# Kernel optimization log

Measured on AMD Instinct MI355X. Metric: run time of the kernel, lower is better.

Reference implementation:

```python
import jax, jax.numpy as jnp
import numpy as np

B, CIN, COUT, K, S, P, D = 4, 128, 128, 3, 1, 1, 1
H = W = 96
MASK_SCALE = 2.0


def setup_inputs() -> dict:
    key = jax.random.key(0)
    k1, k2, k3, k4 = jax.random.split(key, 4)
    x = jax.random.normal(k1, (B, CIN, H, W), jnp.float32)
    weight = jax.random.normal(k2, (COUT, CIN, K, K), jnp.float32) * 0.05
    bias = jax.random.normal(k3, (COUT,), jnp.float32) * 0.05
    # conv_offset_mask: out_channels = deformable_groups*3*K*K = 27, no bias
    w_offmask = jax.random.normal(k4, (3 * K * K, CIN, K, K), jnp.float32) * 0.01
    return {"x": x, "weight": weight, "bias": bias, "w_offmask": w_offmask}


def _bilinear_gather(x, py, px):
    """x: [B,C,H,W]; py,px: [B,K2,Ho,Wo] float sample coords.
    Returns [B,C,K2,Ho,Wo], zero outside image (per-corner validity as in DCNv2)."""
    Bn, C, Hh, Ww = x.shape
    K2, Ho, Wo = py.shape[1], py.shape[2], py.shape[3]
    y0 = jnp.floor(py); x0 = jnp.floor(px)
    ly = py - y0; lx = px - x0
    y0i = y0.astype(jnp.int32); x0i = x0.astype(jnp.int32)
    y1i = y0i + 1; x1i = x0i + 1
    x_flat = x.reshape(Bn, C, Hh * Ww)

    def corner(yi, xi, w):
        valid = (yi >= 0) & (yi < Hh) & (xi >= 0) & (xi < Ww)
        yc = jnp.clip(yi, 0, Hh - 1)
        xc = jnp.clip(xi, 0, Ww - 1)
        idx = (yc * Ww + xc).reshape(Bn, K2 * Ho * Wo)
        v = jnp.take_along_axis(x_flat, idx[:, None, :], axis=2)  # [B,C,K2*Ho*Wo]
        v = v.reshape(Bn, C, K2, Ho, Wo)
        wv = (w * valid.astype(x.dtype))[:, None]  # [B,1,K2,Ho,Wo]
        return v * wv

    out = corner(y0i, x0i, (1 - ly) * (1 - lx))
    out = out + corner(y0i, x1i, (1 - ly) * lx)
    out = out + corner(y1i, x0i, ly * (1 - lx))
    out = out + corner(y1i, x1i, ly * lx)
    return out


def reference(x, weight, bias, w_offmask):
    K2 = K * K
    # offset/mask conv (standard conv, no bias)
    om = jax.lax.conv_general_dilated(
        x, w_offmask, window_strides=(S, S), padding=[(P, P), (P, P)],
        dimension_numbers=("NCHW", "OIHW", "NCHW"))  # [B, 3*K2, Ho, Wo]
    o1 = om[:, :K2]
    o2 = om[:, K2:2 * K2]
    mask = jax.nn.sigmoid(om[:, 2 * K2:]) * MASK_SCALE  # [B,K2,Ho,Wo]
    offset = jnp.concatenate([o1, o2], axis=1)  # [B,2*K2,Ho,Wo]

    Ho, Wo = om.shape[2], om.shape[3]
    ki, kj = jnp.meshgrid(jnp.arange(K), jnp.arange(K), indexing="ij")
    ki = ki.reshape(K2); kj = kj.reshape(K2)
    ho = jnp.arange(Ho); wo = jnp.arange(Wo)
    base_y = (ho[None, :] * S - P + ki[:, None] * D).astype(x.dtype)  # [K2,Ho]
    base_x = (wo[None, :] * S - P + kj[:, None] * D).astype(x.dtype)  # [K2,Wo]
    py = base_y[None, :, :, None] + o1  # [B,K2,Ho,Wo]
    px = base_x[None, :, None, :] + o2

    sampled = _bilinear_gather(x, py, px)            # [B,C,K2,Ho,Wo]
    sampled = sampled * mask[:, None]                # modulation
    wr = weight.reshape(COUT, CIN, K2)
    out = jnp.einsum("ock,bckhw->bohw", wr, sampled) + bias[None, :, None, None]
    return out, offset
```

## Files before the change

kernel.cpp:

```cpp
#include <hip/hip_runtime.h>
#include <math.h>

#define HH 96
#define WW 96
#define HW (96*96)
#define CIN_ 128
#define COUT_ 128
#define OUT_ELEMS (4*128*96*96)
#define TPX 48

#define XT_OFF   0u
#define WBF_OFF  9437184u
#define WOMB_OFF 9732096u

typedef __attribute__((ext_vector_type(8))) short short8v;
typedef __attribute__((ext_vector_type(4))) float float4v;

__device__ __forceinline__ unsigned short f2bf(float f) {
    unsigned u = __builtin_bit_cast(unsigned, f);
    u += 0x7FFFu + ((u >> 16) & 1u);
    return (unsigned short)(u >> 16);
}
__device__ __forceinline__ unsigned rneu(float f) {
    unsigned u = __builtin_bit_cast(unsigned, f);
    return u + 0x7FFFu + ((u >> 16) & 1u);
}
__device__ __forceinline__ unsigned pkbf(float hi, float lo) {
    return __builtin_amdgcn_perm(rneu(hi), rneu(lo), 0x07060302u);
}
__device__ __forceinline__ float bflo(unsigned u) {
    return __builtin_bit_cast(float, u << 16);
}
__device__ __forceinline__ float bfhi(unsigned u) {
    return __builtin_bit_cast(float, u & 0xffff0000u);
}

#define BLOCK_SYNC() do {                                   \
    __builtin_amdgcn_sched_barrier(0);                      \
    asm volatile("s_waitcnt lgkmcnt(0)" ::: "memory");      \
    __builtin_amdgcn_s_barrier();                           \
    __builtin_amdgcn_sched_barrier(0);                      \
} while (0)

__global__ __launch_bounds__(256) void pre_kernel(
    const float* __restrict__ x, const float* __restrict__ w,
    const float* __restrict__ wom, unsigned short* __restrict__ xt,
    unsigned short* __restrict__ wbf, unsigned short* __restrict__ womb)
{
    __shared__ float tile[64][130];
    const int t = threadIdx.x;
    const int f = blockIdx.x;

    if (f < 576) {
        const int g  = (f & 7) * 72 + (f >> 3);
        const int b  = g / 144;
        const int p0 = (g - b * 144) * 64;
#pragma unroll
        for (int j = 0; j < 8; j++) {
            const int i  = j * 256 + t;
            const int c  = i >> 4;
            const int p4 = (i & 15) * 4;
            const float4 v = *(const float4*)(x + ((size_t)(b * CIN_ + c) * HW + p0 + p4));
            tile[p4 + 0][c] = v.x; tile[p4 + 1][c] = v.y;
            tile[p4 + 2][c] = v.z; tile[p4 + 3][c] = v.w;
        }
        __syncthreads();
#pragma unroll
        for (int j = 0; j < 8; j++) {
            const int i   = j * 256 + t;
            const int pxl = i >> 5;
            const int c4  = (i & 31) * 4;
            uint2 v;
            v.x = pkbf(tile[pxl][c4 + 1], tile[pxl][c4 + 0]);
            v.y = pkbf(tile[pxl][c4 + 3], tile[pxl][c4 + 2]);
            *(uint2*)(xt + ((size_t)(b * HW + p0 + pxl) * CIN_ + c4)) = v;
        }
    } else {
        const int i = (f - 576) * 256 + t;
        if (i < COUT_ * 1152) {
            const int oc = i / 1152, r = i - oc * 1152;
            const int kc = r >> 7, c = r & 127;
            wbf[i] = f2bf(w[(size_t)oc * 1152 + c * 9 + kc]);
        } else {
            const int i2 = i - COUT_ * 1152;
            if (i2 < 32 * 1152) {
                const int row = i2 / 1152, r = i2 - row * 1152;
                const int kc = r >> 7, c = r & 127;
                womb[i2] = (row < 27) ? f2bf(wom[(size_t)row * 1152 + c * 9 + kc]) : 0;
            }
        }
    }
}

__global__ __launch_bounds__(512, 6) void dconv_fused(
    const unsigned short* __restrict__ xt, const unsigned short* __restrict__ wbf,
    const unsigned short* __restrict__ womb, const float* __restrict__ bias,
    float* __restrict__ out, float* __restrict__ off_out)
{
    __shared__ int smem[9600];
    int*   sprep  = smem;
    int*   btile0 = smem + 3456;
    int*   btile1 = smem + 6528;
    float* som    = (float*)btile0;

    const int t    = threadIdx.x;
    const int wave = __builtin_amdgcn_readfirstlane(t >> 6);
    const int lane = t & 63;
    const int quad = lane >> 4;
    const int m    = lane & 15;
    const int l32  = lane & 31;
    const int half = lane >> 5;

    const int f  = blockIdx.x;
    const int c  = (f & 7) * 96 + (f >> 3);
    const int b  = c / 192;
    const int p0 = (c - b * 192) * TPX;

    const unsigned short* xtb = xt + (size_t)b * HW * CIN_;

    const int hrow = p0 / 96;
    const int w0   = p0 - hrow * 96;

#pragma unroll
    for (int k = 0; k < 5; k++) {
        const int i = k * 512 + t;
        if (i < 2400) {
            const int row = i >> 4;
            const int ch  = i & 15;
            const int r   = row / 50;
            const int cc  = row - r * 50;
            const int y   = hrow + r - 1;
            const int xx  = w0 + cc - 1;
            uint4 v = make_uint4(0u, 0u, 0u, 0u);
            if (((unsigned)y < 96u) && ((unsigned)xx < 96u))
                v = *(const uint4*)(xtb + (size_t)(y * 96 + xx) * CIN_ + ch * 8);
            *(uint4*)&smem[row * 64 + ((ch ^ (row & 7)) << 2)] = v;
        }
    }
    __syncthreads();

    float4v acc2;
#pragma unroll
    for (int r = 0; r < 4; r++) acc2[r] = 0.f;

    if (wave < 6) {
        const int pxg = wave >> 1;
        const int mt  = wave & 1;
        const int pgl = pxg * 16 + m;

#pragma unroll
        for (int kc = 0; kc < 9; kc++) {
            const int ki = kc / 3, kj = kc - 3 * (kc / 3);
            const int sr = ki * 50 + pgl + kj;
            const short* brow = (const short*)smem + sr * 128;
            const short* abase = (const short*)womb + (size_t)(mt * 16 + m) * 1152 + kc * 128;
#pragma unroll
            for (int kst = 0; kst < 4; kst++) {
                const int c16s = (kst * 4 + quad) ^ (sr & 7);
                const short8v bfv = *(const short8v*)(brow + c16s * 8);
                const short8v av  = *(const short8v*)(abase + kst * 32 + quad * 8);
                acc2 = __builtin_amdgcn_mfma_f32_16x16x32_bf16(av, bfv, acc2, 0, 0, 0);
            }
        }
    }
    __syncthreads();

    if (wave < 6) {
        const int pxg = wave >> 1;
        const int mt  = wave & 1;
        const int pgl = pxg * 16 + m;
        const int pg  = p0 + pgl;
#pragma unroll
        for (int r = 0; r < 4; r++) {
            const int oc = mt * 16 + quad * 4 + r;
            if (oc < 27) som[oc * TPX + pgl] = acc2[r];
            if (oc < 18) off_out[(size_t)(b * 18 + oc) * HW + pg] = acc2[r];
        }
    }
    __syncthreads();

    if (t < 432) {
        const int kc  = t / 48;
        const int pxl = t - kc * 48;
        const int pg  = p0 + pxl;
        const int h   = pg / 96;
        const int w   = pg - h * 96;
        const int ki  = kc / 3, kj = kc - 3 * (kc / 3);

        const float o1 = som[kc * TPX + pxl];
        const float o2 = som[(9 + kc) * TPX + pxl];
        const float mr = som[(18 + kc) * TPX + pxl];
        const float mk = 2.f / (1.f + __expf(-mr));

        const float py = (float)(h - 1 + ki) + o1;
        const float px = (float)(w - 1 + kj) + o2;
        const float y0f = floorf(py), x0f = floorf(px);
        const float ly = py - y0f,    lx = px - x0f;
        const int y0 = (int)y0f, x0 = (int)x0f;
        const int y1 = y0 + 1,   x1 = x0 + 1;

        const float w00 = (1.f - ly) * (1.f - lx), w01 = (1.f - ly) * lx;
        const float w10 = ly * (1.f - lx),         w11 = ly * lx;

        const int yc0 = min(max(y0, 0), HH - 1), yc1 = min(max(y1, 0), HH - 1);
        const int xc0 = min(max(x0, 0), WW - 1), xc1 = min(max(x1, 0), WW - 1);
        const bool vy0 = (y0 >= 0) && (y0 < HH), vy1 = (y1 >= 0) && (y1 < HH);
        const bool vx0 = (x0 >= 0) && (x0 < WW), vx1 = (x1 >= 0) && (x1 < WW);

        sprep[t * 8 + 0] = yc0 * 96 + xc0;
        sprep[t * 8 + 1] = yc0 * 96 + xc1;
        sprep[t * 8 + 2] = yc1 * 96 + xc0;
        sprep[t * 8 + 3] = yc1 * 96 + xc1;
        sprep[t * 8 + 4] = __builtin_bit_cast(int, (vy0 && vx0) ? mk * w00 : 0.f);
        sprep[t * 8 + 5] = __builtin_bit_cast(int, (vy0 && vx1) ? mk * w01 : 0.f);
        sprep[t * 8 + 6] = __builtin_bit_cast(int, (vy1 && vx0) ? mk * w10 : 0.f);
        sprep[t * 8 + 7] = __builtin_bit_cast(int, (vy1 && vx1) ? mk * w11 : 0.f);
    }
    __syncthreads();

    uint2 gbuf[3][4];

#define ISSUE(SL, KCV, ITV) do {                                              \
    const int pxl_ = wave * 6 + (ITV) * 2 + half;                             \
    const int4 id4_ = *(const int4*)&sprep[((KCV) * 48 + pxl_) * 8];          \
    const unsigned co_ = (unsigned)l32 << 3;                                  \
    gbuf[SL][0] = *(const uint2*)((const char*)xtb + (((unsigned)id4_.x << 8) | co_)); \
    gbuf[SL][1] = *(const uint2*)((const char*)xtb + (((unsigned)id4_.y << 8) | co_)); \
    gbuf[SL][2] = *(const uint2*)((const char*)xtb + (((unsigned)id4_.z << 8) | co_)); \
    gbuf[SL][3] = *(const uint2*)((const char*)xtb + (((unsigned)id4_.w << 8) | co_)); \
} while (0)

#define COMBINE(SL, IV) do {                                                  \
    const int pxl_ = wave * 6 + (IV) * 2 + half;                              \
    const float4 w4_ = *(const float4*)&sprep[(kc * 48 + pxl_) * 8 + 4];      \
    const uint2 u0 = gbuf[SL][0], u1 = gbuf[SL][1];                           \
    const uint2 u2 = gbuf[SL][2], u3 = gbuf[SL][3];                           \
    const float v0 = w4_.x*bflo(u0.x) + w4_.y*bflo(u1.x) + w4_.z*bflo(u2.x) + w4_.w*bflo(u3.x); \
    const float v1 = w4_.x*bfhi(u0.x) + w4_.y*bfhi(u1.x) + w4_.z*bfhi(u2.x) + w4_.w*bfhi(u3.x); \
    const float v2 = w4_.x*bflo(u0.y) + w4_.y*bflo(u1.y) + w4_.z*bflo(u2.y) + w4_.w*bflo(u3.y); \
    const float v3 = w4_.x*bfhi(u0.y) + w4_.y*bfhi(u1.y) + w4_.z*bfhi(u2.y) + w4_.w*bfhi(u3.y); \
    uint2 o_;                                                                 \
    o_.x = pkbf(v1, v0);                                                      \
    o_.y = pkbf(v3, v2);                                                      \
    *(uint2*)&bt[pxl_ * 64 + (((l32 >> 1) ^ (pxl_ & 7)) << 2) + ((l32 & 1) << 1)] = o_; \
} while (0)

    float4v acc[3];
#pragma unroll
    for (int j = 0; j < 3; j++)
#pragma unroll
        for (int r = 0; r < 4; r++) acc[j][r] = 0.f;

    ISSUE(0, 0, 0);
    ISSUE(1, 0, 1);
    ISSUE(2, 0, 2);

    for (int kc = 0; kc < 9; kc++) {
        int* bt = (kc & 1) ? btile1 : btile0;

        const short* abase = (const short*)wbf + (size_t)(wave * 16 + m) * 1152 + kc * 128 + quad * 8;
        short8v af[4];
#pragma unroll
        for (int kst = 0; kst < 4; kst++)
            af[kst] = *(const short8v*)(abase + kst * 32);

        COMBINE(0, 0);
        if (kc < 8) ISSUE(0, kc + 1, 0);
        COMBINE(1, 1);
        if (kc < 8) ISSUE(1, kc + 1, 1);
        COMBINE(2, 2);
        if (kc < 8) ISSUE(2, kc + 1, 2);

        BLOCK_SYNC();

#pragma unroll
        for (int kst = 0; kst < 4; kst++) {
#pragma unroll
            for (int nt = 0; nt < 3; nt++) {
                const int pxl = nt * 16 + m;
                const short8v bfv = *(const short8v*)((const short*)bt
                    + 2 * (pxl * 64 + (((kst * 4 + quad) ^ (m & 7)) << 2)));
                acc[nt] = __builtin_amdgcn_mfma_f32_16x16x32_bf16(af[kst], bfv, acc[nt], 0, 0, 0);
            }
        }
    }
#undef ISSUE
#undef COMBINE

#pragma unroll
    for (int r = 0; r < 4; r++) {
        const int oc = wave * 16 + quad * 4 + r;
        const float bv = bias[oc];
#pragma unroll
        for (int nt = 0; nt < 3; nt++)
            out[(size_t)(b * COUT_ + oc) * HW + p0 + nt * 16 + m] = acc[nt][r] + bv;
    }
}

extern "C" void kernel_launch(void* const* d_in, const int* in_sizes, int n_in,
                              void* d_out, int out_size, void* d_ws, size_t ws_size,
                              hipStream_t stream) {
    const float* x      = (const float*)d_in[0];
    const float* weight = (const float*)d_in[1];
    const float* bias   = (const float*)d_in[2];
    const float* wom    = (const float*)d_in[3];

    float* out     = (float*)d_out;
    float* off_out = out + OUT_ELEMS;

    unsigned short* xtb  = (unsigned short*)((char*)d_ws + XT_OFF);
    unsigned short* wbf  = (unsigned short*)((char*)d_ws + WBF_OFF);
    unsigned short* womb = (unsigned short*)((char*)d_ws + WOMB_OFF);

    pre_kernel <<<dim3(1296), 256, 0, stream>>>(x, weight, wom, xtb, wbf, womb);
    dconv_fused<<<dim3(768),  512, 0, stream>>>(xtb, wbf, womb, bias, out, off_out);
}
```

Baseline: 145.9 us.

## Shrink deform-conv tile to 16 pixels with 2-wave blocks and prepacked MFMA weight fragments

The fused deformable conv kernel moves from 512-thread blocks handling 48 pixels to 128-thread blocks handling 16 pixels, launching 2304 blocks instead of 768, each wave now covering 64 output channels over four M-tiles. The pre-kernel now stores both weight matrices in MFMA fragment order, so each lane loads its A operand with one contiguous 16-byte read. The aim is better occupancy and load balance with far less shared memory per block, and the idle-wave phases of the old layout go away. The cost is that each block re-reads all 128x1152 weights for fewer pixels, raising L2 traffic per output, and the halo for the offset conv is recomputed more often.

```diff
diff --git a/kernel.cpp b/kernel.cpp
--- a/kernel.cpp
+++ b/kernel.cpp
@@ -7,7 +7,7 @@
 #define CIN_ 128
 #define COUT_ 128
 #define OUT_ELEMS (4*128*96*96)
-#define TPX 48
+#define TPX 16
 
 #define XT_OFF   0u
 #define WBF_OFF  9437184u
@@ -77,31 +77,41 @@
         }
     } else {
         const int i = (f - 576) * 256 + t;
-        if (i < COUT_ * 1152) {
-            const int oc = i / 1152, r = i - oc * 1152;
-            const int kc = r >> 7, c = r & 127;
+        if (i < 147456) {
+            const int frag = i >> 9;
+            const int lane = (i >> 3) & 63;
+            const int e    = i & 7;
+            const int mt = frag / 36, r = frag - mt * 36;
+            const int kc = r >> 2, kst = r & 3;
+            const int m = lane & 15, quad = lane >> 4;
+            const int oc = mt * 16 + m;
+            const int c  = kst * 32 + quad * 8 + e;
             wbf[i] = f2bf(w[(size_t)oc * 1152 + c * 9 + kc]);
         } else {
-            const int i2 = i - COUT_ * 1152;
-            if (i2 < 32 * 1152) {
-                const int row = i2 / 1152, r = i2 - row * 1152;
-                const int kc = r >> 7, c = r & 127;
-                womb[i2] = (row < 27) ? f2bf(wom[(size_t)row * 1152 + c * 9 + kc]) : 0;
-            }
-        }
-    }
-}
-
-__global__ __launch_bounds__(512, 6) void dconv_fused(
+            const int i2 = i - 147456;
+            const int frag = i2 >> 9;
+            const int lane = (i2 >> 3) & 63;
+            const int e    = i2 & 7;
+            const int mt = frag / 36, r = frag - mt * 36;
+            const int kc = r >> 2, kst = r & 3;
+            const int m = lane & 15, quad = lane >> 4;
+            const int row = mt * 16 + m;
+            const int c   = kst * 32 + quad * 8 + e;
+            womb[i2] = (row < 27) ? f2bf(wom[(size_t)row * 1152 + c * 9 + kc]) : 0;
+        }
+    }
+}
+
+__global__ __launch_bounds__(128, 4) void dconv_small(
     const unsigned short* __restrict__ xt, const unsigned short* __restrict__ wbf,
     const unsigned short* __restrict__ womb, const float* __restrict__ bias,
     float* __restrict__ out, float* __restrict__ off_out)
 {
-    __shared__ int smem[9600];
-    int*   sprep  = smem;
-    int*   btile0 = smem + 3456;
-    int*   btile1 = smem + 6528;
-    float* som    = (float*)btile0;
+    __shared__ int smem[3632];
+    int*   btile0 = smem;
+    int*   btile1 = smem + 1024;
+    int*   sprep  = smem + 2048;
+    float* som    = (float*)(smem + 3200);
 
     const int t    = threadIdx.x;
     const int wave = __builtin_amdgcn_readfirstlane(t >> 6);
@@ -112,24 +122,25 @@
     const int half = lane >> 5;
 
     const int f  = blockIdx.x;
-    const int c  = (f & 7) * 96 + (f >> 3);
-    const int b  = c / 192;
-    const int p0 = (c - b * 192) * TPX;
+    const int c2 = (f & 7) * 288 + (f >> 3);
+    const int b  = c2 / 576;
+    const int p0 = (c2 - b * 576) * TPX;
 
     const unsigned short* xtb = xt + (size_t)b * HW * CIN_;
-
-    const int hrow = p0 / 96;
-    const int w0   = p0 - hrow * 96;
-
-#pragma unroll
-    for (int k = 0; k < 5; k++) {
-        const int i = k * 512 + t;
-        if (i < 2400) {
+    const char* xtB = (const char*)xtb;
+
+    const int h  = p0 / 96;
+    const int w0 = p0 - h * 96;
+
+#pragma unroll
+    for (int k = 0; k < 7; k++) {
+        const int i = k * 128 + t;
+        if (i < 864) {
             const int row = i >> 4;
             const int ch  = i & 15;
-            const int r   = row / 50;
-            const int cc  = row - r * 50;
-            const int y   = hrow + r - 1;
+            const int r   = row / 18;
+            const int cc  = row - r * 18;
+            const int y   = h + r - 1;
             const int xx  = w0 + cc - 1;
             uint4 v = make_uint4(0u, 0u, 0u, 0u);
             if (((unsigned)y < 96u) && ((unsigned)xx < 96u))
@@ -142,97 +153,89 @@
     float4v acc2;
 #pragma unroll
     for (int r = 0; r < 4; r++) acc2[r] = 0.f;
-
-    if (wave < 6) {
-        const int pxg = wave >> 1;
-        const int mt  = wave & 1;
-        const int pgl = pxg * 16 + m;
-
+    {
+        const short* wfB = (const short*)womb + (size_t)wave * 36 * 512 + lane * 8;
 #pragma unroll
         for (int kc = 0; kc < 9; kc++) {
             const int ki = kc / 3, kj = kc - 3 * (kc / 3);
-            const int sr = ki * 50 + pgl + kj;
+            const int sr = ki * 18 + m + kj;
             const short* brow = (const short*)smem + sr * 128;
-            const short* abase = (const short*)womb + (size_t)(mt * 16 + m) * 1152 + kc * 128;
 #pragma unroll
             for (int kst = 0; kst < 4; kst++) {
                 const int c16s = (kst * 4 + quad) ^ (sr & 7);
                 const short8v bfv = *(const short8v*)(brow + c16s * 8);
-                const short8v av  = *(const short8v*)(abase + kst * 32 + quad * 8);
+                const short8v av  = *(const short8v*)(wfB + (kc * 4 + kst) * 512);
                 acc2 = __builtin_amdgcn_mfma_f32_16x16x32_bf16(av, bfv, acc2, 0, 0, 0);
             }
         }
     }
     __syncthreads();
 
-    if (wave < 6) {
-        const int pxg = wave >> 1;
-        const int mt  = wave & 1;
-        const int pgl = pxg * 16 + m;
-        const int pg  = p0 + pgl;
+    {
 #pragma unroll
         for (int r = 0; r < 4; r++) {
-            const int oc = mt * 16 + quad * 4 + r;
-            if (oc < 27) som[oc * TPX + pgl] = acc2[r];
-            if (oc < 18) off_out[(size_t)(b * 18 + oc) * HW + pg] = acc2[r];
+            const int oc = wave * 16 + quad * 4 + r;
+            if (oc < 27) som[oc * 16 + m] = acc2[r];
+            if (oc < 18) off_out[(size_t)(b * 18 + oc) * HW + p0 + m] = acc2[r];
         }
     }
     __syncthreads();
 
-    if (t < 432) {
-        const int kc  = t / 48;
-        const int pxl = t - kc * 48;
-        const int pg  = p0 + pxl;
-        const int h   = pg / 96;
-        const int w   = pg - h * 96;
-        const int ki  = kc / 3, kj = kc - 3 * (kc / 3);
-
-        const float o1 = som[kc * TPX + pxl];
-        const float o2 = som[(9 + kc) * TPX + pxl];
-        const float mr = som[(18 + kc) * TPX + pxl];
-        const float mk = 2.f / (1.f + __expf(-mr));
-
-        const float py = (float)(h - 1 + ki) + o1;
-        const float px = (float)(w - 1 + kj) + o2;
-        const float y0f = floorf(py), x0f = floorf(px);
-        const float ly = py - y0f,    lx = px - x0f;
-        const int y0 = (int)y0f, x0 = (int)x0f;
-        const int y1 = y0 + 1,   x1 = x0 + 1;
-
-        const float w00 = (1.f - ly) * (1.f - lx), w01 = (1.f - ly) * lx;
-        const float w10 = ly * (1.f - lx),         w11 = ly * lx;
-
-        const int yc0 = min(max(y0, 0), HH - 1), yc1 = min(max(y1, 0), HH - 1);
-        const int xc0 = min(max(x0, 0), WW - 1), xc1 = min(max(x1, 0), WW - 1);
-        const bool vy0 = (y0 >= 0) && (y0 < HH), vy1 = (y1 >= 0) && (y1 < HH);
-        const bool vx0 = (x0 >= 0) && (x0 < WW), vx1 = (x1 >= 0) && (x1 < WW);
-
-        sprep[t * 8 + 0] = yc0 * 96 + xc0;
-        sprep[t * 8 + 1] = yc0 * 96 + xc1;
-        sprep[t * 8 + 2] = yc1 * 96 + xc0;
-        sprep[t * 8 + 3] = yc1 * 96 + xc1;
-        sprep[t * 8 + 4] = __builtin_bit_cast(int, (vy0 && vx0) ? mk * w00 : 0.f);
-        sprep[t * 8 + 5] = __builtin_bit_cast(int, (vy0 && vx1) ? mk * w01 : 0.f);
-        sprep[t * 8 + 6] = __builtin_bit_cast(int, (vy1 && vx0) ? mk * w10 : 0.f);
-        sprep[t * 8 + 7] = __builtin_bit_cast(int, (vy1 && vx1) ? mk * w11 : 0.f);
+#pragma unroll
+    for (int k = 0; k < 2; k++) {
+        const int it = k * 128 + t;
+        if (it < 144) {
+            const int kc = it >> 4;
+            const int px = it & 15;
+            const int ki = kc / 3, kj = kc - 3 * (kc / 3);
+
+            const float o1 = som[kc * 16 + px];
+            const float o2 = som[(9 + kc) * 16 + px];
+            const float mr = som[(18 + kc) * 16 + px];
+            const float mk = 2.f / (1.f + __expf(-mr));
+
+            const float py  = (float)(h - 1 + ki) + o1;
+            const float pxf = (float)(w0 + px - 1 + kj) + o2;
+            const float y0f = floorf(py), x0f = floorf(pxf);
+            const float ly = py - y0f,    lx = pxf - x0f;
+            const int y0 = (int)y0f, x0 = (int)x0f;
+            const int y1 = y0 + 1,   x1 = x0 + 1;
+
+            const float w00 = (1.f - ly) * (1.f - lx), w01 = (1.f - ly) * lx;
+            const float w10 = ly * (1.f - lx),         w11 = ly * lx;
+
+            const int yc0 = min(max(y0, 0), HH - 1), yc1 = min(max(y1, 0), HH - 1);
+            const int xc0 = min(max(x0, 0), WW - 1), xc1 = min(max(x1, 0), WW - 1);
+            const bool vy0 = (y0 >= 0) && (y0 < HH), vy1 = (y1 >= 0) && (y1 < HH);
+            const bool vx0 = (x0 >= 0) && (x0 < WW), vx1 = (x1 >= 0) && (x1 < WW);
+
+            sprep[it * 8 + 0] = yc0 * 96 + xc0;
+            sprep[it * 8 + 1] = yc0 * 96 + xc1;
+            sprep[it * 8 + 2] = yc1 * 96 + xc0;
+            sprep[it * 8 + 3] = yc1 * 96 + xc1;
+            sprep[it * 8 + 4] = __builtin_bit_cast(int, (vy0 && vx0) ? mk * w00 : 0.f);
+            sprep[it * 8 + 5] = __builtin_bit_cast(int, (vy0 && vx1) ? mk * w01 : 0.f);
+            sprep[it * 8 + 6] = __builtin_bit_cast(int, (vy1 && vx0) ? mk * w10 : 0.f);
+            sprep[it * 8 + 7] = __builtin_bit_cast(int, (vy1 && vx1) ? mk * w11 : 0.f);
+        }
     }
     __syncthreads();
 
-    uint2 gbuf[3][4];
+    uint2 gbuf[4][4];
 
 #define ISSUE(SL, KCV, ITV) do {                                              \
-    const int pxl_ = wave * 6 + (ITV) * 2 + half;                             \
-    const int4 id4_ = *(const int4*)&sprep[((KCV) * 48 + pxl_) * 8];          \
+    const int pxl_ = wave * 8 + (ITV) * 2 + half;                             \
+    const int4 id4_ = *(const int4*)&sprep[((KCV) * 16 + pxl_) * 8];          \
     const unsigned co_ = (unsigned)l32 << 3;                                  \
-    gbuf[SL][0] = *(const uint2*)((const char*)xtb + (((unsigned)id4_.x << 8) | co_)); \
-    gbuf[SL][1] = *(const uint2*)((const char*)xtb + (((unsigned)id4_.y << 8) | co_)); \
-    gbuf[SL][2] = *(const uint2*)((const char*)xtb + (((unsigned)id4_.z << 8) | co_)); \
-    gbuf[SL][3] = *(const uint2*)((const char*)xtb + (((unsigned)id4_.w << 8) | co_)); \
+    gbuf[SL][0] = *(const uint2*)(xtB + (((unsigned)id4_.x << 8) | co_));     \
+    gbuf[SL][1] = *(const uint2*)(xtB + (((unsigned)id4_.y << 8) | co_));     \
+    gbuf[SL][2] = *(const uint2*)(xtB + (((unsigned)id4_.z << 8) | co_));     \
+    gbuf[SL][3] = *(const uint2*)(xtB + (((unsigned)id4_.w << 8) | co_));     \
 } while (0)
 
 #define COMBINE(SL, IV) do {                                                  \
-    const int pxl_ = wave * 6 + (IV) * 2 + half;                              \
-    const float4 w4_ = *(const float4*)&sprep[(kc * 48 + pxl_) * 8 + 4];      \
+    const int pxl_ = wave * 8 + (IV) * 2 + half;                              \
+    const float4 w4_ = *(const float4*)&sprep[(kc * 16 + pxl_) * 8 + 4];      \
     const uint2 u0 = gbuf[SL][0], u1 = gbuf[SL][1];                           \
     const uint2 u2 = gbuf[SL][2], u3 = gbuf[SL][3];                           \
     const float v0 = w4_.x*bflo(u0.x) + w4_.y*bflo(u1.x) + w4_.z*bflo(u2.x) + w4_.w*bflo(u3.x); \
@@ -245,24 +248,21 @@
     *(uint2*)&bt[pxl_ * 64 + (((l32 >> 1) ^ (pxl_ & 7)) << 2) + ((l32 & 1) << 1)] = o_; \
 } while (0)
 
-    float4v acc[3];
-#pragma unroll
-    for (int j = 0; j < 3; j++)
+    float4v acc[4];
+#pragma unroll
+    for (int j = 0; j < 4; j++)
 #pragma unroll
         for (int r = 0; r < 4; r++) acc[j][r] = 0.f;
+
+    const char* wfrag = (const char*)wbf + ((size_t)wave * 4 * 36) * 1024 + lane * 16;
 
     ISSUE(0, 0, 0);
     ISSUE(1, 0, 1);
     ISSUE(2, 0, 2);
+    ISSUE(3, 0, 3);
 
     for (int kc = 0; kc < 9; kc++) {
         int* bt = (kc & 1) ? btile1 : btile0;
-
-        const short* abase = (const short*)wbf + (size_t)(wave * 16 + m) * 1152 + kc * 128 + quad * 8;
-        short8v af[4];
-#pragma unroll
-        for (int kst = 0; kst < 4; kst++)
-            af[kst] = *(const short8v*)(abase + kst * 32);
 
         COMBINE(0, 0);
         if (kc < 8) ISSUE(0, kc + 1, 0);
@@ -270,17 +270,20 @@
         if (kc < 8) ISSUE(1, kc + 1, 1);
         COMBINE(2, 2);
         if (kc < 8) ISSUE(2, kc + 1, 2);
+        COMBINE(3, 3);
+        if (kc < 8) ISSUE(3, kc + 1, 3);
 
         BLOCK_SYNC();
 
 #pragma unroll
         for (int kst = 0; kst < 4; kst++) {
-#pragma unroll
-            for (int nt = 0; nt < 3; nt++) {
-                const int pxl = nt * 16 + m;
-                const short8v bfv = *(const short8v*)((const short*)bt
-                    + 2 * (pxl * 64 + (((kst * 4 + quad) ^ (m & 7)) << 2)));
-                acc[nt] = __builtin_amdgcn_mfma_f32_16x16x32_bf16(af[kst], bfv, acc[nt], 0, 0, 0);
+            const short8v bfv = *(const short8v*)((const short*)bt
+                + 2 * (m * 64 + (((kst * 4 + quad) ^ (m & 7)) << 2)));
+#pragma unroll
+            for (int mt = 0; mt < 4; mt++) {
+                const short8v af = *(const short8v*)(wfrag
+                    + ((size_t)(mt * 36 + kc * 4 + kst)) * 1024);
+                acc[mt] = __builtin_amdgcn_mfma_f32_16x16x32_bf16(af, bfv, acc[mt], 0, 0, 0);
             }
         }
     }
@@ -288,12 +291,12 @@
 #undef COMBINE
 
 #pragma unroll
-    for (int r = 0; r < 4; r++) {
-        const int oc = wave * 16 + quad * 4 + r;
-        const float bv = bias[oc];
-#pragma unroll
-        for (int nt = 0; nt < 3; nt++)
-            out[(size_t)(b * COUT_ + oc) * HW + p0 + nt * 16 + m] = acc[nt][r] + bv;
+    for (int mt = 0; mt < 4; mt++) {
+#pragma unroll
+        for (int r = 0; r < 4; r++) {
+            const int oc = wave * 64 + mt * 16 + quad * 4 + r;
+            out[(size_t)(b * COUT_ + oc) * HW + p0 + m] = acc[mt][r] + bias[oc];
+        }
     }
 }
 
@@ -313,5 +316,5 @@
     unsigned short* womb = (unsigned short*)((char*)d_ws + WOMB_OFF);
 
     pre_kernel <<<dim3(1296), 256, 0, stream>>>(x, weight, wom, xtb, wbf, womb);
-    dconv_fused<<<dim3(768),  512, 0, stream>>>(xtb, wbf, womb, bias, out, off_out);
-}
+    dconv_small<<<dim3(2304), 128, 0, stream>>>(xtb, wbf, womb, bias, out, off_out);
+}
```

Result: faster. 131.9 us (-9.6%).
